# Performance work log

Hardware: AMD Instinct MI355X
Metric: run time of the kernel (lower is better)

The kernel has to match this reference:

```python
import jax, jax.numpy as jnp
import numpy as np

N = 20000   # nodes
E = 160000  # edges
C = 512     # input_size / channels
D = 16      # edge_size
H = 256     # hidden_size
EPS = 1e-5  # BatchNorm eps (eval mode, init running stats: mean=0, var=1)


def setup_inputs() -> dict:
    key = jax.random.key(0)
    ks = jax.random.split(key, 24)
    w = lambda k, shape: (jax.random.normal(k, shape, jnp.float32) * 0.02)
    inp = {
        "x": jax.random.normal(ks[0], (N, C), jnp.float32),
        "edge_index": jax.random.randint(ks[1], (2, E), 0, N, jnp.int32),
        "edge_attr": jax.random.normal(ks[2], (E, D), jnp.float32),
        "goal_feat": jax.random.normal(ks[3], (N, C), jnp.float32),
        # CGConv 1
        "Wf1": w(ks[4], (2 * C + D, C)), "bf1": jnp.zeros((C,), jnp.float32),
        "Ws1": w(ks[5], (2 * C + D, C)), "bs1": jnp.zeros((C,), jnp.float32),
        "g1": jnp.ones((C,), jnp.float32), "be1": jnp.zeros((C,), jnp.float32),
        # CGConv 2
        "Wf2": w(ks[6], (2 * C + D, C)), "bf2": jnp.zeros((C,), jnp.float32),
        "Ws2": w(ks[7], (2 * C + D, C)), "bs2": jnp.zeros((C,), jnp.float32),
        "g2": jnp.ones((C,), jnp.float32), "be2": jnp.zeros((C,), jnp.float32),
        # GCNConv 3, 4
        "W3": w(ks[8], (C, H)), "b3": jnp.zeros((H,), jnp.float32),
        "W4": w(ks[9], (H, H)), "b4": jnp.zeros((H,), jnp.float32),
        # distance MLP: Lin(H+C -> C), ReLU, Lin(C -> 1)
        "Wd1": w(ks[10], (H + C, C)), "bd1": jnp.zeros((C,), jnp.float32),
        "Wd2": w(ks[11], (C, 1)), "bd2": jnp.zeros((1,), jnp.float32),
    }
    return inp


def cg_conv(x, src, dst, edge_attr, Wf, bf, Ws, bs, gamma, beta):
    # PyG CGConv: z = x_i || x_j || e;  m = sigmoid(lin_f(z)) * softplus(lin_s(z))
    # aggr='add' at targets, BatchNorm (eval, init stats), residual.
    z = jnp.concatenate([x[dst], x[src], edge_attr], axis=-1)  # [E, 2C+D]
    m = jax.nn.sigmoid(z @ Wf + bf) * jax.nn.softplus(z @ Ws + bs)  # [E, C]
    agg = jax.ops.segment_sum(m, dst, num_segments=N)  # [N, C]
    agg = agg * (gamma / jnp.sqrt(1.0 + EPS)) + beta   # BN eval (mean=0, var=1)
    return agg + x


def gcn_conv(x, src, dst, W, b):
    # PyG GCNConv with add_self_loops=True, normalize=True
    h = x @ W  # [N, out]
    loop = jnp.arange(N, dtype=src.dtype)
    s = jnp.concatenate([src, loop])
    d = jnp.concatenate([dst, loop])
    deg = jax.ops.segment_sum(jnp.ones_like(d, jnp.float32), d, num_segments=N)
    dinv = jnp.where(deg > 0, jax.lax.rsqrt(jnp.maximum(deg, 1.0)), 0.0)
    norm = dinv[s] * dinv[d]  # [E+N]
    out = jax.ops.segment_sum(norm[:, None] * h[s], d, num_segments=N)
    return out + b


def reference(x, edge_index, edge_attr, goal_feat,
              Wf1, bf1, Ws1, bs1, g1, be1,
              Wf2, bf2, Ws2, bs2, g2, be2,
              W3, b3, W4, b4, Wd1, bd1, Wd2, bd2):
    src = edge_index[0]  # x_j (source)
    dst = edge_index[1]  # x_i (target)
    h = jax.nn.relu(cg_conv(x, src, dst, edge_attr, Wf1, bf1, Ws1, bs1, g1, be1))
    h = jax.nn.relu(cg_conv(h, src, dst, edge_attr, Wf2, bf2, Ws2, bs2, g2, be2))
    h = jax.nn.relu(gcn_conv(h, src, dst, W3, b3))
    h = jax.nn.relu(gcn_conv(h, src, dst, W4, b4))
    z = jnp.concatenate([h, goal_feat], axis=1)  # [N, H+C]
    pred_dist = jax.nn.relu(z @ Wd1 + bd1) @ Wd2 + bd2  # [N, 1]
    return pred_dist, h
```

## Files before the change

### kernel.cpp

```cpp
#include <hip/hip_runtime.h>
#include <stdint.h>

#define NNODES 20000
#define NEDGES 160000
#define NPAD   20096

typedef float f32x4 __attribute__((ext_vector_type(4)));
typedef float f32x2 __attribute__((ext_vector_type(2)));
typedef short s16x8 __attribute__((ext_vector_type(8)));
typedef unsigned int u32x4 __attribute__((ext_vector_type(4)));
typedef _Float16 h16x2 __attribute__((ext_vector_type(2)));

__device__ __forceinline__ float b2f(unsigned short b) {
    unsigned int u = ((unsigned int)b) << 16;
    return __builtin_bit_cast(float, u);
}
__device__ __forceinline__ unsigned short f2b(float f) {
    unsigned int u = __builtin_bit_cast(unsigned int, f);
    unsigned int r = (u + 0x7FFFu + ((u >> 16) & 1u)) >> 16;
    return (unsigned short)r;
}
__device__ __forceinline__ f32x2 unpack2(unsigned int u) {
    f32x2 r;
    r.x = __builtin_bit_cast(float, u << 16);
    r.y = __builtin_bit_cast(float, u & 0xFFFF0000u);
    return r;
}
__device__ __forceinline__ unsigned int packh2(float a, float b) {
    h16x2 h = { (_Float16)a, (_Float16)b };
    return __builtin_bit_cast(unsigned int, h);
}
__device__ __forceinline__ float dot2h(unsigned int a, unsigned int b, float c) {
#if __has_builtin(__builtin_amdgcn_fdot2)
    return __builtin_amdgcn_fdot2(__builtin_bit_cast(h16x2, a),
                                  __builtin_bit_cast(h16x2, b), c, false);
#else
    float d;
    asm("v_dot2_f32_f16 %0, %1, %2, %3" : "=v"(d) : "v"(a), "v"(b), "v"(c));
    return d;
#endif
}

__global__ __launch_bounds__(256) void gemm_bt_kernel(
    const unsigned short* __restrict__ A,
    const unsigned short* __restrict__ BT,
    float* __restrict__ Cf,
    unsigned short* __restrict__ Cb,
    int M, int N, int K,
    const float* __restrict__ bias)
{
    __shared__ unsigned short As[128 * 32];
    __shared__ unsigned short Bs[128 * 32];
    const int tid  = threadIdx.x;
    const int wid  = tid >> 6;
    const int lane = tid & 63;
    const int bm = blockIdx.x * 128;
    const int bn = blockIdx.y * 128;
    const int wm = (wid & 1) * 64;
    const int wn = (wid >> 1) * 64;

    f32x4 acc[4][4];
#pragma unroll
    for (int i = 0; i < 4; i++)
#pragma unroll
        for (int j = 0; j < 4; j++) acc[i][j] = {0.f, 0.f, 0.f, 0.f};

    for (int k0 = 0; k0 < K; k0 += 32) {
#pragma unroll
        for (int r = 0; r < 2; r++) {
            int flat = r * 256 + tid;
            int row  = flat >> 2;
            int part = flat & 3;
            const unsigned short* ga = A  + (size_t)(bm + row) * K + k0 + part * 8;
            const unsigned short* gb = BT + (size_t)(bn + row) * K + k0 + part * 8;
            __builtin_amdgcn_global_load_lds(
                (const __attribute__((address_space(1))) unsigned int*)ga,
                (__attribute__((address_space(3))) unsigned int*)&As[flat * 8], 16, 0, 0);
            __builtin_amdgcn_global_load_lds(
                (const __attribute__((address_space(1))) unsigned int*)gb,
                (__attribute__((address_space(3))) unsigned int*)&Bs[flat * 8], 16, 0, 0);
        }
        __syncthreads();

        const int kq = (lane >> 4) * 8;
        const int rl = lane & 15;
        s16x8 af[4], bfr[4];
#pragma unroll
        for (int mi = 0; mi < 4; mi++)
            af[mi] = *(const s16x8*)&As[(wm + mi * 16 + rl) * 32 + kq];
#pragma unroll
        for (int ni = 0; ni < 4; ni++)
            bfr[ni] = *(const s16x8*)&Bs[(wn + ni * 16 + rl) * 32 + kq];
#pragma unroll
        for (int mi = 0; mi < 4; mi++)
#pragma unroll
            for (int ni = 0; ni < 4; ni++)
                acc[mi][ni] = __builtin_amdgcn_mfma_f32_16x16x32_bf16(
                    af[mi], bfr[ni], acc[mi][ni], 0, 0, 0);
        __syncthreads();
    }

    const int cl = lane & 15;
    const int rq = (lane >> 4) * 4;
#pragma unroll
    for (int mi = 0; mi < 4; mi++)
#pragma unroll
        for (int ni = 0; ni < 4; ni++)
#pragma unroll
            for (int r = 0; r < 4; r++) {
                int row = bm + wm + mi * 16 + rq + r;
                int col = bn + wn + ni * 16 + cl;
                float v = acc[mi][ni][r];
                if (Cb) {
                    if (bias) v = fmaxf(v + bias[col], 0.f);
                    Cb[(size_t)row * N + col] = f2b(v);
                } else {
                    Cf[(size_t)row * N + col] = v;
                }
            }
}

__global__ void count_kernel(const int* __restrict__ ei, int* __restrict__ counts) {
    int e = blockIdx.x * blockDim.x + threadIdx.x;
    if (e < NEDGES) atomicAdd(&counts[ei[NEDGES + e]], 1);
}

__global__ __launch_bounds__(1024) void scan_kernel(const int* __restrict__ counts,
                                                    int* __restrict__ row_ptr)
{
    __shared__ int sdata[1024];
    const int t = threadIdx.x;
    int vals[20];
    const int base = t * 20;
    int lsum = 0;
#pragma unroll
    for (int j = 0; j < 20; j++) {
        int idx = base + j;
        int v = (idx < NNODES) ? counts[idx] : 0;
        vals[j] = v; lsum += v;
    }
    sdata[t] = lsum;
    __syncthreads();
    for (int off = 1; off < 1024; off <<= 1) {
        int v = (t >= off) ? sdata[t - off] : 0;
        __syncthreads();
        sdata[t] += v;
        __syncthreads();
    }
    int run = sdata[t] - lsum;
#pragma unroll
    for (int j = 0; j < 20; j++) {
        int idx = base + j;
        if (idx < NNODES) row_ptr[idx] = run;
        run += vals[j];
    }
    if (t == 1023) row_ptr[NNODES] = sdata[1023];
}

__global__ void fill_kernel(const int* __restrict__ ei,
                            const int* __restrict__ row_ptr,
                            int* __restrict__ cursor,
                            int* __restrict__ csr_src,
                            int* __restrict__ csr_eid)
{
    int e = blockIdx.x * blockDim.x + threadIdx.x;
    if (e >= NEDGES) return;
    int dst = ei[NEDGES + e];
    int p = row_ptr[dst] + atomicAdd(&cursor[dst], 1);
    csr_src[p] = ei[e];
    csr_eid[p] = e;
}

__global__ void dinv_kernel(const int* __restrict__ row_ptr, float* __restrict__ dinv) {
    int i = blockIdx.x * blockDim.x + threadIdx.x;
    if (i < NNODES) {
        int deg = row_ptr[i + 1] - row_ptr[i] + 1;
        dinv[i] = rsqrtf((float)deg);
    }
}

__global__ void pad_copy_kernel(const float* __restrict__ src,
                                unsigned short* __restrict__ dst,
                                int valid_rows, int cols, long total)
{
    long idx = (long)blockIdx.x * blockDim.x + threadIdx.x;
    if (idx >= total) return;
    int n = (int)(idx / cols);
    dst[idx] = (n < valid_rows) ? f2b(src[idx]) : (unsigned short)0;
}

__global__ void pack_cgw_kernel(const float* __restrict__ Wf,
                                const float* __restrict__ Ws,
                                unsigned short* __restrict__ out)
{
    int idx = blockIdx.x * blockDim.x + threadIdx.x;
    if (idx >= 2048 * 512) return;
    int j = idx >> 9;
    int k = idx & 511;
    int half = (j >= 1024);
    int jj = j & 1023;
    int c  = (jj >> 2) * 2 + (jj & 1);
    int fs = (jj >> 1) & 1;
    const float* W = fs ? Ws : Wf;
    float v = W[(size_t)(half ? 512 + k : k) * 512 + c];
    out[idx] = f2b(v);
}

__global__ void pack_t_kernel(const float* __restrict__ W,
                              unsigned short* __restrict__ WT,
                              int K, int Nout)
{
    long idx = (long)blockIdx.x * blockDim.x + threadIdx.x;
    if (idx >= (long)K * Nout) return;
    int j = (int)(idx / K);
    int k = (int)(idx % K);
    WT[idx] = f2b(W[(size_t)k * Nout + j]);
}

__global__ void pack_we_kernel(const float* __restrict__ Wf,
                               const float* __restrict__ Ws,
                               unsigned int* __restrict__ out)
{
    int idx = blockIdx.x * blockDim.x + threadIdx.x;
    if (idx >= 8192) return;
    int q  = idx & 3;
    int c2 = (idx >> 2) & 255;
    int k  = idx >> 10;
    const float* W = (q >> 1) ? Ws : Wf;
    int c = c2 * 2 + (q & 1);
    float v0 = W[(size_t)(1024 + 2 * k) * 512 + c];
    float v1 = W[(size_t)(1024 + 2 * k + 1) * 512 + c];
    out[idx] = packh2(v0, v1);
}

__global__ void pack_ea_kernel(const int* __restrict__ csr_eid,
                               const float* __restrict__ ea,
                               unsigned int* __restrict__ out)
{
    int idx = blockIdx.x * blockDim.x + threadIdx.x;
    if (idx >= NEDGES * 8) return;
    int i = idx >> 3;
    int j = idx & 7;
    int eid = csr_eid[i];
    out[idx] = packh2(ea[(size_t)eid * 16 + 2 * j], ea[(size_t)eid * 16 + 2 * j + 1]);
}

#define CG_NPB 2

#define CG_LOADE(q_, a0_, a1_, idx) do {                                       \
    int sx_ = __builtin_amdgcn_readfirstlane(csr_src[idx]);                    \
    q_  = *(const uint2*)(P + (size_t)sx_ * 2048 + 1024 + c0 * 2);             \
    a0_ = eapk[(size_t)(idx) * 2];                                             \
    a1_ = eapk[(size_t)(idx) * 2 + 1];                                         \
} while (0)

#define CG_COMP(q_, a0_, a1_) do {                                             \
    float f0 = baseF.x, f1 = baseF.y, s0 = baseS.x, s1 = baseS.y;              \
    _Pragma("unroll")                                                          \
    for (int k = 0; k < 4; k++) {                                              \
        f0 = dot2h(a0_[k], w[k][0], f0);                                       \
        f1 = dot2h(a0_[k], w[k][1], f1);                                       \
        s0 = dot2h(a0_[k], w[k][2], s0);                                       \
        s1 = dot2h(a0_[k], w[k][3], s1);                                       \
    }                                                                          \
    _Pragma("unroll")                                                          \
    for (int k = 0; k < 4; k++) {                                              \
        f0 = dot2h(a1_[k], w[4 + k][0], f0);                                   \
        f1 = dot2h(a1_[k], w[4 + k][1], f1);                                   \
        s0 = dot2h(a1_[k], w[4 + k][2], s0);                                   \
        s1 = dot2h(a1_[k], w[4 + k][3], s1);                                   \
    }                                                                          \
    f32x2 pf = unpack2(q_.x);                                                  \
    f32x2 ps = unpack2(q_.y);                                                  \
    f0 += pf.x; f1 += pf.y; s0 += ps.x; s1 += ps.y;                            \
    float sp0 = __logf(1.f + __expf(s0));                                      \
    float sp1 = __logf(1.f + __expf(s1));                                      \
    float sg0 = __builtin_amdgcn_rcpf(1.f + __expf(-f0));                      \
    float sg1 = __builtin_amdgcn_rcpf(1.f + __expf(-f1));                      \
    acc.x = fmaf(sp0, sg0, acc.x);                                             \
    acc.y = fmaf(sp1, sg1, acc.y);                                             \
} while (0)

__global__ __launch_bounds__(256, 1) void cg_gather_kernel(
    const unsigned short* __restrict__ P,
    const int* __restrict__ row_ptr,
    const int* __restrict__ csr_src,
    const u32x4* __restrict__ wE,
    const u32x4* __restrict__ eapk,
    const float* __restrict__ bfv,
    const float* __restrict__ bsv,
    const float* __restrict__ g,
    const float* __restrict__ be,
    const float* __restrict__ xresf,
    const unsigned short* __restrict__ xresb,
    unsigned short* __restrict__ hout)
{
    const int tid = threadIdx.x;
    const int c0  = tid * 2;
    const int nbase = blockIdx.x * CG_NPB;

    u32x4 w[8];
#pragma unroll
    for (int k = 0; k < 8; k++) w[k] = wE[k * 256 + tid];

    const f32x2 bfx = *(const f32x2*)&bfv[c0];
    const f32x2 bsx = *(const f32x2*)&bsv[c0];
    const f32x2 gv  = *(const f32x2*)&g[c0];
    const f32x2 bev = *(const f32x2*)&be[c0];
    const float rs = rsqrtf(1.f + 1e-5f);

    for (int n = nbase; n < nbase + CG_NPB; n++) {
        if (n >= NNODES) {
            *(unsigned int*)&hout[(size_t)n * 512 + c0] = 0;
            continue;
        }
        const unsigned short* Pd = P + (size_t)n * 2048;
        const uint2 qb = *(const uint2*)(Pd + c0 * 2);
        const f32x2 baseF = unpack2(qb.x) + bfx;
        const f32x2 baseS = unpack2(qb.y) + bsx;

        f32x2 acc = {0.f, 0.f};
        const int i0 = __builtin_amdgcn_readfirstlane(row_ptr[n]);
        const int i1 = __builtin_amdgcn_readfirstlane(row_ptr[n + 1]);

        if (i0 < i1) {
            uint2 qA = {}, qB = {};
            u32x4 aA0 = {}, aA1 = {}, aB0 = {}, aB1 = {};
            CG_LOADE(qA, aA0, aA1, i0);
            if (i0 + 1 < i1) CG_LOADE(qB, aB0, aB1, i0 + 1);
            int i = i0;
            while (i < i1) {
                CG_COMP(qA, aA0, aA1);
                if (i + 2 < i1) CG_LOADE(qA, aA0, aA1, i + 2);
                if (++i >= i1) break;
                CG_COMP(qB, aB0, aB1);
                if (i + 2 < i1) CG_LOADE(qB, aB0, aB1, i + 2);
                ++i;
            }
        }

        f32x2 res;
        if (xresf) {
            res = *(const f32x2*)&xresf[(size_t)n * 512 + c0];
        } else {
            res = unpack2(*(const unsigned int*)&xresb[(size_t)n * 512 + c0]);
        }
        float v0 = fmaxf(acc.x * (gv.x * rs) + bev.x + res.x, 0.f);
        float v1 = fmaxf(acc.y * (gv.y * rs) + bev.y + res.y, 0.f);
        unsigned int packed = (unsigned int)f2b(v0) | ((unsigned int)f2b(v1) << 16);
        *(unsigned int*)&hout[(size_t)n * 512 + c0] = packed;
    }
}

__global__ __launch_bounds__(256) void gcn_gather_kernel(
    const unsigned short* __restrict__ pre,
    const int* __restrict__ row_ptr,
    const int* __restrict__ csr_src,
    const float* __restrict__ dinv,
    const float* __restrict__ b,
    unsigned short* __restrict__ hout,
    float* __restrict__ doutf)
{
    const int tid = threadIdx.x;
    const int n = blockIdx.x * 2 + (tid >> 7);
    const int c = (tid & 127) * 2;
    if (n >= NNODES) {
        if (n < NPAD) *(unsigned int*)&hout[(size_t)n * 256 + c] = 0;
        return;
    }
    const float din = dinv[n];
    f32x2 acc = {0.f, 0.f};
    const int i0 = __builtin_amdgcn_readfirstlane(row_ptr[n]);
    const int i1 = __builtin_amdgcn_readfirstlane(row_ptr[n + 1]);
    if (i0 < i1) {
        float dvA = 0.f, dvB = 0.f;
        unsigned int pvA = 0, pvB = 0;
        {
            int sx = __builtin_amdgcn_readfirstlane(csr_src[i0]);
            dvA = dinv[sx];
            pvA = *(const unsigned int*)&pre[(size_t)sx * 256 + c];
        }
        if (i0 + 1 < i1) {
            int sx = __builtin_amdgcn_readfirstlane(csr_src[i0 + 1]);
            dvB = dinv[sx];
            pvB = *(const unsigned int*)&pre[(size_t)sx * 256 + c];
        }
        int i = i0;
        while (i < i1) {
            {
                f32x2 p = unpack2(pvA);
                acc.x = fmaf(dvA, p.x, acc.x);
                acc.y = fmaf(dvA, p.y, acc.y);
            }
            if (i + 2 < i1) {
                int sx = __builtin_amdgcn_readfirstlane(csr_src[i + 2]);
                dvA = dinv[sx];
                pvA = *(const unsigned int*)&pre[(size_t)sx * 256 + c];
            }
            if (++i >= i1) break;
            {
                f32x2 p = unpack2(pvB);
                acc.x = fmaf(dvB, p.x, acc.x);
                acc.y = fmaf(dvB, p.y, acc.y);
            }
            if (i + 2 < i1) {
                int sx = __builtin_amdgcn_readfirstlane(csr_src[i + 2]);
                dvB = dinv[sx];
                pvB = *(const unsigned int*)&pre[(size_t)sx * 256 + c];
            }
            ++i;
        }
    }
    f32x2 self = unpack2(*(const unsigned int*)&pre[(size_t)n * 256 + c]);
    const f32x2 bv = *(const f32x2*)&b[c];
    float v0 = fmaxf(fmaf(acc.x, din, din * din * self.x) + bv.x, 0.f);
    float v1 = fmaxf(fmaf(acc.y, din, din * din * self.y) + bv.y, 0.f);
    *(unsigned int*)&hout[(size_t)n * 256 + c] =
        (unsigned int)f2b(v0) | ((unsigned int)f2b(v1) << 16);
    if (doutf) {
        f32x2 vv = {v0, v1};
        *(f32x2*)&doutf[(size_t)n * 256 + c] = vv;
    }
}

__global__ void build_zc_kernel(const unsigned short* __restrict__ h4,
                                const float* __restrict__ goal,
                                unsigned short* __restrict__ zc)
{
    long idx = (long)blockIdx.x * blockDim.x + threadIdx.x;
    if (idx >= (long)NPAD * 768) return;
    int n = (int)(idx / 768);
    int c = (int)(idx % 768);
    unsigned short v = 0;
    if (n < NNODES)
        v = (c < 256) ? h4[(size_t)n * 256 + c]
                      : f2b(goal[(size_t)n * 512 + (c - 256)]);
    zc[idx] = v;
}

__global__ __launch_bounds__(256) void final_dot_kernel(
    const unsigned short* __restrict__ t,
    const float* __restrict__ Wd2,
    const float* __restrict__ bd2,
    float* __restrict__ pred)
{
    const int lane = threadIdx.x & 63;
    const int wid  = threadIdx.x >> 6;
    float w[8];
#pragma unroll
    for (int i = 0; i < 8; i++) w[i] = Wd2[lane * 8 + i];
    const float bd = bd2[0];
    for (int n = blockIdx.x * 4 + wid; n < NNODES; n += gridDim.x * 4) {
        const unsigned short* tp = t + (size_t)n * 512 + lane * 8;
        float s = 0.f;
#pragma unroll
        for (int i = 0; i < 8; i++) s = fmaf(b2f(tp[i]), w[i], s);
#pragma unroll
        for (int off = 32; off; off >>= 1) s += __shfl_xor(s, off, 64);
        if (lane == 0) pred[n] = s + bd;
    }
}

extern "C" void kernel_launch(void* const* d_in, const int* in_sizes, int n_in,
                              void* d_out, int out_size, void* d_ws, size_t ws_size,
                              hipStream_t stream)
{
    (void)in_sizes; (void)n_in; (void)out_size; (void)ws_size;
    const float* x    = (const float*)d_in[0];
    const int*   ei   = (const int*)d_in[1];
    const float* ea   = (const float*)d_in[2];
    const float* goal = (const float*)d_in[3];
    const float* Wf1  = (const float*)d_in[4];
    const float* bf1  = (const float*)d_in[5];
    const float* Ws1  = (const float*)d_in[6];
    const float* bs1  = (const float*)d_in[7];
    const float* g1   = (const float*)d_in[8];
    const float* be1  = (const float*)d_in[9];
    const float* Wf2  = (const float*)d_in[10];
    const float* bf2  = (const float*)d_in[11];
    const float* Ws2  = (const float*)d_in[12];
    const float* bs2  = (const float*)d_in[13];
    const float* g2   = (const float*)d_in[14];
    const float* be2  = (const float*)d_in[15];
    const float* W3   = (const float*)d_in[16];
    const float* b3   = (const float*)d_in[17];
    const float* W4   = (const float*)d_in[18];
    const float* b4   = (const float*)d_in[19];
    const float* Wd1  = (const float*)d_in[20];
    const float* bd1  = (const float*)d_in[21];
    const float* Wd2  = (const float*)d_in[22];
    const float* bd2  = (const float*)d_in[23];
    float* outp = (float*)d_out;

    char* ws = (char*)d_ws;
    size_t off = 0;
    auto alloc = [&](size_t bytes) -> char* {
        char* p = ws + off;
        off += (bytes + 255) & ~(size_t)255;
        return p;
    };
    unsigned short* P     = (unsigned short*)alloc((size_t)NPAD * 2048 * 2);
    unsigned short* bufA  = (unsigned short*)alloc((size_t)NPAD * 512 * 2);
    unsigned short* bufB  = (unsigned short*)alloc((size_t)NPAD * 512 * 2);
    unsigned short* bufC  = (unsigned short*)alloc((size_t)NPAD * 512 * 2);
    unsigned short* wpack = (unsigned short*)alloc((size_t)2048 * 512 * 2);
    int*            counts  = (int*)alloc((size_t)NNODES * 4);
    int*            row_ptr = (int*)alloc((size_t)(NNODES + 1) * 4);
    int*            csr_src = (int*)alloc((size_t)NEDGES * 4);
    int*            csr_eid = (int*)alloc((size_t)NEDGES * 4);
    float*          dinv    = (float*)alloc((size_t)NNODES * 4);
    unsigned int*   wEbuf   = (unsigned int*)alloc((size_t)8192 * 4);
    unsigned int*   eapk    = (unsigned int*)alloc((size_t)NEDGES * 8 * 4);

    unsigned short* xpad  = bufA;
    unsigned short* h1    = bufB;
    unsigned short* h2    = bufA;
    unsigned short* pre_b = bufB;
    unsigned short* h3    = bufC;
    unsigned short* h4    = bufA;
    unsigned short* zc    = P;
    unsigned short* tb    = P + (size_t)NPAD * 1024;

    const int B = 256;

    hipMemsetAsync(counts, 0, (size_t)NNODES * 4, stream);
    count_kernel<<<(NEDGES + B - 1) / B, B, 0, stream>>>(ei, counts);
    scan_kernel<<<1, 1024, 0, stream>>>(counts, row_ptr);
    hipMemsetAsync(counts, 0, (size_t)NNODES * 4, stream);
    fill_kernel<<<(NEDGES + B - 1) / B, B, 0, stream>>>(ei, row_ptr, counts, csr_src, csr_eid);
    dinv_kernel<<<(NNODES + B - 1) / B, B, 0, stream>>>(row_ptr, dinv);
    pack_ea_kernel<<<(NEDGES * 8 + B - 1) / B, B, 0, stream>>>(csr_eid, ea, eapk);

    {
        long tot = (long)NPAD * 512;
        pad_copy_kernel<<<(unsigned)((tot + B - 1) / B), B, 0, stream>>>(x, xpad, NNODES, 512, tot);
    }

    dim3 gBig(NPAD / 128, 2048 / 128);

    pack_cgw_kernel<<<(2048 * 512 + B - 1) / B, B, 0, stream>>>(Wf1, Ws1, wpack);
    pack_we_kernel<<<(8192 + B - 1) / B, B, 0, stream>>>(Wf1, Ws1, wEbuf);
    gemm_bt_kernel<<<gBig, B, 0, stream>>>(xpad, wpack, nullptr, P, NPAD, 2048, 512, nullptr);
    cg_gather_kernel<<<NPAD / CG_NPB, B, 0, stream>>>(P, row_ptr, csr_src,
                                                      (const u32x4*)wEbuf, (const u32x4*)eapk,
                                                      bf1, bs1, g1, be1,
                                                      x, nullptr, h1);

    pack_cgw_kernel<<<(2048 * 512 + B - 1) / B, B, 0, stream>>>(Wf2, Ws2, wpack);
    gemm_bt_kernel<<<gBig, B, 0, stream>>>(h1, wpack, nullptr, P, NPAD, 2048, 512, nullptr);
    pack_we_kernel<<<(8192 + B - 1) / B, B, 0, stream>>>(Wf2, Ws2, wEbuf);
    cg_gather_kernel<<<NPAD / CG_NPB, B, 0, stream>>>(P, row_ptr, csr_src,
                                                      (const u32x4*)wEbuf, (const u32x4*)eapk,
                                                      bf2, bs2, g2, be2,
                                                      nullptr, h1, h2);

    pack_t_kernel<<<(256 * 512 + B - 1) / B, B, 0, stream>>>(W3, wpack, 512, 256);
    gemm_bt_kernel<<<dim3(NPAD / 128, 2), B, 0, stream>>>(h2, wpack, nullptr, pre_b, NPAD, 256, 512, nullptr);
    gcn_gather_kernel<<<NPAD / 2, B, 0, stream>>>(pre_b, row_ptr, csr_src, dinv, b3, h3, (float*)nullptr);

    pack_t_kernel<<<(256 * 256 + B - 1) / B, B, 0, stream>>>(W4, wpack, 256, 256);
    gemm_bt_kernel<<<dim3(NPAD / 128, 2), B, 0, stream>>>(h3, wpack, nullptr, pre_b, NPAD, 256, 256, nullptr);
    gcn_gather_kernel<<<NPAD / 2, B, 0, stream>>>(pre_b, row_ptr, csr_src, dinv, b4, h4, outp + NNODES);

    build_zc_kernel<<<(unsigned)(((long)NPAD * 768 + B - 1) / B), B, 0, stream>>>(h4, goal, zc);
    pack_t_kernel<<<(512 * 768 + B - 1) / B, B, 0, stream>>>(Wd1, wpack, 768, 512);
    gemm_bt_kernel<<<dim3(NPAD / 128, 4), B, 0, stream>>>(zc, wpack, nullptr, tb, NPAD, 512, 768, bd1);
    final_dot_kernel<<<512, B, 0, stream>>>(tb, Wd2, bd2, outp);
}
```

Baseline: 794.0 us.

## Double GEMM K-tile with XOR-swizzled LDS and deepen gather prefetch pipelines

The bf16 MFMA GEMM now stages a 64-wide K slice per iteration instead of 32. An XOR swizzle on the 16-byte chunk index avoids LDS bank conflicts and halves the barriers per K. The CGConv gather handles 4 nodes per block with a 3-deep edge prefetch ring instead of 2. The GCN gather assigns one wave per node with 4 channels per lane and a 3-deep prefetch. These aim to hide gather latency and cut barrier overhead, at the cost of more LDS and registers per block, which may lower occupancy.

```diff
diff --git a/kernel.cpp b/kernel.cpp
--- a/kernel.cpp
+++ b/kernel.cpp
@@ -49,8 +49,8 @@
     int M, int N, int K,
     const float* __restrict__ bias)
 {
-    __shared__ unsigned short As[128 * 32];
-    __shared__ unsigned short Bs[128 * 32];
+    __shared__ unsigned short As[128 * 64];
+    __shared__ unsigned short Bs[128 * 64];
     const int tid  = threadIdx.x;
     const int wid  = tid >> 6;
     const int lane = tid & 63;
@@ -65,14 +65,15 @@
 #pragma unroll
         for (int j = 0; j < 4; j++) acc[i][j] = {0.f, 0.f, 0.f, 0.f};
 
-    for (int k0 = 0; k0 < K; k0 += 32) {
-#pragma unroll
-        for (int r = 0; r < 2; r++) {
+    for (int k0 = 0; k0 < K; k0 += 64) {
+#pragma unroll
+        for (int r = 0; r < 4; r++) {
             int flat = r * 256 + tid;
-            int row  = flat >> 2;
-            int part = flat & 3;
-            const unsigned short* ga = A  + (size_t)(bm + row) * K + k0 + part * 8;
-            const unsigned short* gb = BT + (size_t)(bn + row) * K + k0 + part * 8;
+            int row  = flat >> 3;
+            int part = flat & 7;
+            int pg   = part ^ (row & 7);
+            const unsigned short* ga = A  + (size_t)(bm + row) * K + k0 + pg * 8;
+            const unsigned short* gb = BT + (size_t)(bn + row) * K + k0 + pg * 8;
             __builtin_amdgcn_global_load_lds(
                 (const __attribute__((address_space(1))) unsigned int*)ga,
                 (__attribute__((address_space(3))) unsigned int*)&As[flat * 8], 16, 0, 0);
@@ -82,21 +83,30 @@
         }
         __syncthreads();
 
-        const int kq = (lane >> 4) * 8;
-        const int rl = lane & 15;
-        s16x8 af[4], bfr[4];
-#pragma unroll
-        for (int mi = 0; mi < 4; mi++)
-            af[mi] = *(const s16x8*)&As[(wm + mi * 16 + rl) * 32 + kq];
-#pragma unroll
-        for (int ni = 0; ni < 4; ni++)
-            bfr[ni] = *(const s16x8*)&Bs[(wn + ni * 16 + rl) * 32 + kq];
-#pragma unroll
-        for (int mi = 0; mi < 4; mi++)
-#pragma unroll
-            for (int ni = 0; ni < 4; ni++)
-                acc[mi][ni] = __builtin_amdgcn_mfma_f32_16x16x32_bf16(
-                    af[mi], bfr[ni], acc[mi][ni], 0, 0, 0);
+        const int kq8 = lane >> 4;
+        const int rl  = lane & 15;
+#pragma unroll
+        for (int kk = 0; kk < 2; kk++) {
+            s16x8 af[4], bfr[4];
+#pragma unroll
+            for (int mi = 0; mi < 4; mi++) {
+                int row = wm + mi * 16 + rl;
+                int slot = (kk * 4 + kq8) ^ (row & 7);
+                af[mi] = *(const s16x8*)&As[row * 64 + slot * 8];
+            }
+#pragma unroll
+            for (int ni = 0; ni < 4; ni++) {
+                int row = wn + ni * 16 + rl;
+                int slot = (kk * 4 + kq8) ^ (row & 7);
+                bfr[ni] = *(const s16x8*)&Bs[row * 64 + slot * 8];
+            }
+#pragma unroll
+            for (int mi = 0; mi < 4; mi++)
+#pragma unroll
+                for (int ni = 0; ni < 4; ni++)
+                    acc[mi][ni] = __builtin_amdgcn_mfma_f32_16x16x32_bf16(
+                        af[mi], bfr[ni], acc[mi][ni], 0, 0, 0);
+        }
         __syncthreads();
     }
 
@@ -245,7 +255,7 @@
     out[idx] = packh2(ea[(size_t)eid * 16 + 2 * j], ea[(size_t)eid * 16 + 2 * j + 1]);
 }
 
-#define CG_NPB 2
+#define CG_NPB 4
 
 #define CG_LOADE(q_, a0_, a1_, idx) do {                                       \
     int sx_ = __builtin_amdgcn_readfirstlane(csr_src[idx]);                    \
@@ -320,22 +330,25 @@
         const f32x2 baseS = unpack2(qb.y) + bsx;
 
         f32x2 acc = {0.f, 0.f};
-        const int i0 = __builtin_amdgcn_readfirstlane(row_ptr[n]);
-        const int i1 = __builtin_amdgcn_readfirstlane(row_ptr[n + 1]);
+        const int i0 = row_ptr[n], i1 = row_ptr[n + 1];
 
         if (i0 < i1) {
-            uint2 qA = {}, qB = {};
-            u32x4 aA0 = {}, aA1 = {}, aB0 = {}, aB1 = {};
+            uint2 qA = {}, qB = {}, qC = {};
+            u32x4 aA0 = {}, aA1 = {}, aB0 = {}, aB1 = {}, aC0 = {}, aC1 = {};
             CG_LOADE(qA, aA0, aA1, i0);
             if (i0 + 1 < i1) CG_LOADE(qB, aB0, aB1, i0 + 1);
+            if (i0 + 2 < i1) CG_LOADE(qC, aC0, aC1, i0 + 2);
             int i = i0;
-            while (i < i1) {
+            while (true) {
                 CG_COMP(qA, aA0, aA1);
-                if (i + 2 < i1) CG_LOADE(qA, aA0, aA1, i + 2);
+                if (i + 3 < i1) CG_LOADE(qA, aA0, aA1, i + 3);
                 if (++i >= i1) break;
                 CG_COMP(qB, aB0, aB1);
-                if (i + 2 < i1) CG_LOADE(qB, aB0, aB1, i + 2);
-                ++i;
+                if (i + 3 < i1) CG_LOADE(qB, aB0, aB1, i + 3);
+                if (++i >= i1) break;
+                CG_COMP(qC, aC0, aC1);
+                if (i + 3 < i1) CG_LOADE(qC, aC0, aC1, i + 3);
+                if (++i >= i1) break;
             }
         }
 
@@ -361,65 +374,68 @@
     unsigned short* __restrict__ hout,
     float* __restrict__ doutf)
 {
-    const int tid = threadIdx.x;
-    const int n = blockIdx.x * 2 + (tid >> 7);
-    const int c = (tid & 127) * 2;
+    const int tid  = threadIdx.x;
+    const int lane = tid & 63;
+    const int n = blockIdx.x * 4 + (tid >> 6);
+    const int c = lane * 4;
     if (n >= NNODES) {
-        if (n < NPAD) *(unsigned int*)&hout[(size_t)n * 256 + c] = 0;
+        if (n < NPAD) { uint2 z = {0u, 0u}; *(uint2*)&hout[(size_t)n * 256 + c] = z; }
         return;
     }
     const float din = dinv[n];
-    f32x2 acc = {0.f, 0.f};
-    const int i0 = __builtin_amdgcn_readfirstlane(row_ptr[n]);
-    const int i1 = __builtin_amdgcn_readfirstlane(row_ptr[n + 1]);
+    f32x4 acc = {0.f, 0.f, 0.f, 0.f};
+    const int i0 = row_ptr[n], i1 = row_ptr[n + 1];
+
+#define GCN_LOADE(dv_, pv_, idx) do {                                          \
+    int sx_ = __builtin_amdgcn_readfirstlane(csr_src[idx]);                    \
+    dv_ = dinv[sx_];                                                           \
+    pv_ = *(const uint2*)&pre[(size_t)sx_ * 256 + c];                          \
+} while (0)
+
+#define GCN_COMP(dv_, pv_) do {                                                \
+    f32x2 p0 = unpack2(pv_.x);                                                 \
+    f32x2 p1 = unpack2(pv_.y);                                                 \
+    acc.x = fmaf(dv_, p0.x, acc.x);                                            \
+    acc.y = fmaf(dv_, p0.y, acc.y);                                            \
+    acc.z = fmaf(dv_, p1.x, acc.z);                                            \
+    acc.w = fmaf(dv_, p1.y, acc.w);                                            \
+} while (0)
+
     if (i0 < i1) {
-        float dvA = 0.f, dvB = 0.f;
-        unsigned int pvA = 0, pvB = 0;
-        {
-            int sx = __builtin_amdgcn_readfirstlane(csr_src[i0]);
-            dvA = dinv[sx];
-            pvA = *(const unsigned int*)&pre[(size_t)sx * 256 + c];
+        float dvA = 0.f, dvB = 0.f, dvC = 0.f;
+        uint2 pvA = {}, pvB = {}, pvC = {};
+        GCN_LOADE(dvA, pvA, i0);
+        if (i0 + 1 < i1) GCN_LOADE(dvB, pvB, i0 + 1);
+        if (i0 + 2 < i1) GCN_LOADE(dvC, pvC, i0 + 2);
+        int i = i0;
+        while (true) {
+            GCN_COMP(dvA, pvA);
+            if (i + 3 < i1) GCN_LOADE(dvA, pvA, i + 3);
+            if (++i >= i1) break;
+            GCN_COMP(dvB, pvB);
+            if (i + 3 < i1) GCN_LOADE(dvB, pvB, i + 3);
+            if (++i >= i1) break;
+            GCN_COMP(dvC, pvC);
+            if (i + 3 < i1) GCN_LOADE(dvC, pvC, i + 3);
+            if (++i >= i1) break;
         }
-        if (i0 + 1 < i1) {
-            int sx = __builtin_amdgcn_readfirstlane(csr_src[i0 + 1]);
-            dvB = dinv[sx];
-            pvB = *(const unsigned int*)&pre[(size_t)sx * 256 + c];
-        }
-        int i = i0;
-        while (i < i1) {
-            {
-                f32x2 p = unpack2(pvA);
-                acc.x = fmaf(dvA, p.x, acc.x);
-                acc.y = fmaf(dvA, p.y, acc.y);
-            }
-            if (i + 2 < i1) {
-                int sx = __builtin_amdgcn_readfirstlane(csr_src[i + 2]);
-                dvA = dinv[sx];
-                pvA = *(const unsigned int*)&pre[(size_t)sx * 256 + c];
-            }
-            if (++i >= i1) break;
-            {
-                f32x2 p = unpack2(pvB);
-                acc.x = fmaf(dvB, p.x, acc.x);
-                acc.y = fmaf(dvB, p.y, acc.y);
-            }
-            if (i + 2 < i1) {
-                int sx = __builtin_amdgcn_readfirstlane(csr_src[i + 2]);
-                dvB = dinv[sx];
-                pvB = *(const unsigned int*)&pre[(size_t)sx * 256 + c];
-            }
-            ++i;
-        }
-    }
-    f32x2 self = unpack2(*(const unsigned int*)&pre[(size_t)n * 256 + c]);
-    const f32x2 bv = *(const f32x2*)&b[c];
-    float v0 = fmaxf(fmaf(acc.x, din, din * din * self.x) + bv.x, 0.f);
-    float v1 = fmaxf(fmaf(acc.y, din, din * din * self.y) + bv.y, 0.f);
-    *(unsigned int*)&hout[(size_t)n * 256 + c] =
-        (unsigned int)f2b(v0) | ((unsigned int)f2b(v1) << 16);
+    }
+    uint2 sv = *(const uint2*)&pre[(size_t)n * 256 + c];
+    f32x2 s0 = unpack2(sv.x);
+    f32x2 s1 = unpack2(sv.y);
+    const f32x4 bv = *(const f32x4*)&b[c];
+    const float d2 = din * din;
+    float v0 = fmaxf(fmaf(acc.x, din, d2 * s0.x) + bv.x, 0.f);
+    float v1 = fmaxf(fmaf(acc.y, din, d2 * s0.y) + bv.y, 0.f);
+    float v2 = fmaxf(fmaf(acc.z, din, d2 * s1.x) + bv.z, 0.f);
+    float v3 = fmaxf(fmaf(acc.w, din, d2 * s1.y) + bv.w, 0.f);
+    uint2 o;
+    o.x = (unsigned int)f2b(v0) | ((unsigned int)f2b(v1) << 16);
+    o.y = (unsigned int)f2b(v2) | ((unsigned int)f2b(v3) << 16);
+    *(uint2*)&hout[(size_t)n * 256 + c] = o;
     if (doutf) {
-        f32x2 vv = {v0, v1};
-        *(f32x2*)&doutf[(size_t)n * 256 + c] = vv;
+        f32x4 vv = {v0, v1, v2, v3};
+        *(f32x4*)&doutf[(size_t)n * 256 + c] = vv;
     }
 }
 
@@ -556,11 +572,11 @@
 
     pack_t_kernel<<<(256 * 512 + B - 1) / B, B, 0, stream>>>(W3, wpack, 512, 256);
     gemm_bt_kernel<<<dim3(NPAD / 128, 2), B, 0, stream>>>(h2, wpack, nullptr, pre_b, NPAD, 256, 512, nullptr);
-    gcn_gather_kernel<<<NPAD / 2, B, 0, stream>>>(pre_b, row_ptr, csr_src, dinv, b3, h3, (float*)nullptr);
+    gcn_gather_kernel<<<NPAD / 4, B, 0, stream>>>(pre_b, row_ptr, csr_src, dinv, b3, h3, (float*)nullptr);
 
     pack_t_kernel<<<(256 * 256 + B - 1) / B, B, 0, stream>>>(W4, wpack, 256, 256);
     gemm_bt_kernel<<<dim3(NPAD / 128, 2), B, 0, stream>>>(h3, wpack, nullptr, pre_b, NPAD, 256, 256, nullptr);
-    gcn_gather_kernel<<<NPAD / 2, B, 0, stream>>>(pre_b, row_ptr, csr_src, dinv, b4, h4, outp + NNODES);
+    gcn_gather_kernel<<<NPAD / 4, B, 0, stream>>>(pre_b, row_ptr, csr_src, dinv, b4, h4, outp + NNODES);
 
     build_zc_kernel<<<(unsigned)(((long)NPAD * 768 + B - 1) / B), B, 0, stream>>>(h4, goal, zc);
     pack_t_kernel<<<(512 * 768 + B - 1) / B, B, 0, stream>>>(Wd1, wpack, 768, 512);
```

Measured after the change: 813.1 us. 1.02x slower.
